# Optimization experiments

Measured on AMD Instinct MI355X. Metric: run time of the kernel, lower is better.

## Reference

```python
import jax, jax.numpy as jnp
import numpy as np

K = 6  # kernel size (square)
_LP = (K - 1) // 2          # 2: PyTorch 'same' left pad for even kernel
_RP = (K - 1) - _LP         # 3: right pad


@jax.custom_vjp
def spike_boxcar(x):
    # Heaviside step with boxcar surrogate gradient (DECOLLE-style)
    return (x > 0).astype(x.dtype)

def _spike_fwd(x):
    return spike_boxcar(x), x

def _spike_bwd(x, g):
    # grad is passed through only where -0.5 < x <= 0.5
    return (jnp.where((x > -0.5) & (x <= 0.5), g, jnp.zeros_like(g)),)

spike_boxcar.defvjp(_spike_fwd, _spike_bwd)


def setup_inputs() -> dict:
    key = jax.random.key(0)
    kx, kw = jax.random.split(key)
    B, Cin, H, W, T = 32, 1, 64, 64, 100
    Cout = 8
    x = jax.random.normal(kx, (B, Cin, H, W, T), dtype=jnp.float32)
    # Conv2d default init: U(-1/sqrt(fan_in), 1/sqrt(fan_in)), fan_in = Cin*K*K
    bound = 1.0 / np.sqrt(Cin * K * K)
    w = jax.random.uniform(kw, (Cout, Cin, K, K), dtype=jnp.float32,
                           minval=-bound, maxval=bound)
    thresh = jnp.full((1,), 0.8, dtype=jnp.float32)
    return {"x": x, "w": w, "thresh": thresh}


def reference(x, w, thresh):
    B, Cin, H, W, T = x.shape
    Cout = w.shape[0]
    # Batch all timesteps into one conv call (conv is independent of state)
    xt = jnp.moveaxis(x, -1, 0).reshape(T * B, Cin, H, W)
    Wx = jax.lax.conv_general_dilated(
        xt, w, window_strides=(1, 1),
        padding=[(_LP, _RP), (_LP, _RP)],
        dimension_numbers=("NCHW", "OIHW", "NCHW"),
    ).reshape(T, B, Cout, H, W)

    ut0 = jnp.zeros((B, Cout, H, W), dtype=x.dtype)
    st0 = jnp.zeros_like(ut0)

    def step(carry, wx):
        ut, st = carry
        ut = ut - st * thresh[0] + wx
        st = spike_boxcar(ut)
        return (ut, st), st

    _, s = jax.lax.scan(step, (ut0, st0), Wx)  # s: [T, B, Cout, H, W]
    return jnp.moveaxis(s, 0, -1)              # [B, Cout, H, W, T]
```

## Files before the change

kernel.cpp:

```cpp
#include <hip/hip_runtime.h>

#define HH 64
#define WW 64
#define TT 100
#define CO 8
#define COB 4
#define KS 6
#define LP 2
#define HALO 21
#define NSITE 441
#define NGMAX 7

__device__ __forceinline__ float stepu(float u, float s, float th, float wx) {
    return __fadd_rn(__fsub_rn(u, __fmul_rn(s, th)), wx);
}

template<int T0, int TC>
__device__ __forceinline__ void process_chunk(
    const float* __restrict__ xb,
    float4* __restrict__ xs, const float (*wds)[CO],
    int tid, int r, int c, int h0, int w0, int co0, float th,
    float* ut, float* sprev, unsigned* bw )
{
    constexpr int NG = TC / 4;

    for (int i = tid; i < NSITE * NG; i += 256) {
        const int s  = i / NG;
        const int tg = i - s * NG;
        const int hr = s / HALO;
        const int hc = s - hr * HALO;
        const int hh = h0 - LP + hr;
        const int ww = w0 - LP + hc;
        float4 v = make_float4(0.f, 0.f, 0.f, 0.f);
        if ((unsigned)hh < (unsigned)HH && (unsigned)ww < (unsigned)WW)
            v = *(const float4*)(xb + ((size_t)hh * WW + ww) * TT + T0 + tg * 4);
        xs[tg * NSITE + s] = v;
    }
    __syncthreads();

    unsigned cb[COB];
#pragma unroll
    for (int j = 0; j < COB; ++j) cb[j] = 0u;

    for (int tg = 0; tg < NG; ++tg) {
        float4 wx[COB];
#pragma unroll
        for (int j = 0; j < COB; ++j) wx[j] = make_float4(0.f, 0.f, 0.f, 0.f);
#pragma unroll
        for (int kh = 0; kh < KS; ++kh) {
#pragma unroll
            for (int kw = 0; kw < KS; ++kw) {
                const float4 xv = xs[tg * NSITE + (r + kh) * HALO + (c + kw)];
                const int tap = kh * KS + kw;
#pragma unroll
                for (int j = 0; j < COB; ++j) {
                    const float wd = wds[tap][co0 + j];
                    wx[j].x = __fmaf_rn(wd, xv.x, wx[j].x);
                    wx[j].y = __fmaf_rn(wd, xv.y, wx[j].y);
                    wx[j].z = __fmaf_rn(wd, xv.z, wx[j].z);
                    wx[j].w = __fmaf_rn(wd, xv.w, wx[j].w);
                }
            }
        }
        const int sh = tg * 4;
#pragma unroll
        for (int j = 0; j < COB; ++j) {
            float u = ut[j], s = sprev[j];
            unsigned m = 0u;
            u = stepu(u, s, th, wx[j].x); s = (u > 0.f) ? 1.f : 0.f; m |= (u > 0.f) ? 1u : 0u;
            u = stepu(u, s, th, wx[j].y); s = (u > 0.f) ? 1.f : 0.f; m |= (u > 0.f) ? 2u : 0u;
            u = stepu(u, s, th, wx[j].z); s = (u > 0.f) ? 1.f : 0.f; m |= (u > 0.f) ? 4u : 0u;
            u = stepu(u, s, th, wx[j].w); s = (u > 0.f) ? 1.f : 0.f; m |= (u > 0.f) ? 8u : 0u;
            ut[j] = u; sprev[j] = s;
            cb[j] |= m << sh;
        }
    }
    __syncthreads();

    constexpr int W0 = T0 / 32;
    constexpr int S  = T0 % 32;
#pragma unroll
    for (int j = 0; j < COB; ++j) {
        bw[j * 4 + W0] |= cb[j] << S;
        if constexpr (S + TC > 32)
            bw[j * 4 + W0 + 1] |= cb[j] >> ((32 - S) & 31);
    }
}

__global__ __launch_bounds__(256, 2)
void sconv2d_spike_kernel(const float* __restrict__ x,
                          const float* __restrict__ wgt,
                          const float* __restrict__ thresh,
                          float* __restrict__ out)
{
    __shared__ float4   xs[NGMAX * NSITE];
    __shared__ float    wds[KS * KS][CO];
    __shared__ unsigned stg[256][5];

    const int tid = threadIdx.x;
    for (int i = tid; i < KS * KS * CO; i += 256) {
        const int co  = i / (KS * KS);
        const int tap = i - co * (KS * KS);
        wds[tap][co] = wgt[co * (KS * KS) + tap];
    }
    const float th = thresh[0];

    const int blk  = blockIdx.x;
    const int b    = blk >> 5;
    const int rest = blk & 31;
    const int tb   = rest >> 1;
    const int co0  = (rest & 1) * COB;
    const int h0   = (tb >> 2) << 4;
    const int w0   = (tb & 3) << 4;
    const int r    = tid >> 4;
    const int c    = tid & 15;

    const float* xb   = x   + (size_t)b * (HH * WW * TT);
    float*       outb = out + (size_t)b * (CO * HH * WW * TT);

    float ut[COB], sprev[COB];
    unsigned bw[COB * 4];
#pragma unroll
    for (int j = 0; j < COB; ++j) { ut[j] = 0.f; sprev[j] = 0.f; }
#pragma unroll
    for (int i = 0; i < COB * 4; ++i) bw[i] = 0u;

    process_chunk< 0, 28>(xb, xs, wds, tid, r, c, h0, w0, co0, th, ut, sprev, bw);
    process_chunk<28, 28>(xb, xs, wds, tid, r, c, h0, w0, co0, th, ut, sprev, bw);
    process_chunk<56, 28>(xb, xs, wds, tid, r, c, h0, w0, co0, th, ut, sprev, bw);
    process_chunk<84, 16>(xb, xs, wds, tid, r, c, h0, w0, co0, th, ut, sprev, bw);

#pragma unroll
    for (int j = 0; j < COB; ++j) {
        const int co = co0 + j;
        stg[tid][0] = bw[j * 4 + 0];
        stg[tid][1] = bw[j * 4 + 1];
        stg[tid][2] = bw[j * 4 + 2];
        stg[tid][3] = bw[j * 4 + 3];
        __syncthreads();
#pragma unroll
        for (int k = 0; k < 25; ++k) {
            const int idx = tid + k * 256;
            const int u   = idx / 25;
            const int tt  = (idx - u * 25) * 4;
            const unsigned bs = stg[u][tt >> 5] >> (tt & 31);
            float4 v;
            v.x = (float)( bs        & 1u);
            v.y = (float)((bs >> 1)  & 1u);
            v.z = (float)((bs >> 2)  & 1u);
            v.w = (float)((bs >> 3)  & 1u);
            const int rr = u >> 4, cc = u & 15;
            *(float4*)(outb + (((size_t)co * HH + (h0 + rr)) * WW + (w0 + cc)) * TT + tt) = v;
        }
        __syncthreads();
    }
}

extern "C" void kernel_launch(void* const* d_in, const int* in_sizes, int n_in,
                              void* d_out, int out_size, void* d_ws, size_t ws_size,
                              hipStream_t stream) {
    const float* x      = (const float*)d_in[0];
    const float* wgt    = (const float*)d_in[1];
    const float* thresh = (const float*)d_in[2];
    float* out = (float*)d_out;

    dim3 grid(32 * 16 * 2);
    dim3 block(256);
    sconv2d_spike_kernel<<<grid, block, 0, stream>>>(x, wgt, thresh, out);
}
```

Baseline: 548.1 us.

## Double-buffer input via global_load_lds and compute all output channels per block

Each block now handles all 8 output channels, halving the grid and avoiding the duplicate halo loads of the old two-channel-group split. Input chunks of 20 timesteps are staged with asynchronous global-to-LDS loads into two ping-pong buffers, so the next chunk's transfer overlaps the current chunk's convolution. Out-of-bounds halo sites are handled by clamped addresses plus per-thread row and column validity masks multiplied into the inputs, instead of branches. The cost is more registers per thread (8 channel accumulators), fewer blocks to fill the machine, and reuse of the LDS input buffer for spike-bit staging.

Result: slower. 1.098 ms (+100.3%).

```diff
diff --git a/kernel.cpp b/kernel.cpp
--- a/kernel.cpp
+++ b/kernel.cpp
@@ -4,86 +4,92 @@
 #define WW 64
 #define TT 100
 #define CO 8
-#define COB 4
 #define KS 6
 #define LP 2
 #define HALO 21
 #define NSITE 441
-#define NGMAX 7
+#define NG 5
+#define SLOT_PAD 2304
 
 __device__ __forceinline__ float stepu(float u, float s, float th, float wx) {
     return __fadd_rn(__fsub_rn(u, __fmul_rn(s, th)), wx);
 }
 
-template<int T0, int TC>
-__device__ __forceinline__ void process_chunk(
-    const float* __restrict__ xb,
-    float4* __restrict__ xs, const float (*wds)[CO],
-    int tid, int r, int c, int h0, int w0, int co0, float th,
-    float* ut, float* sprev, unsigned* bw )
+#define GLDS16(gp, lp) \
+    __builtin_amdgcn_global_load_lds((const __attribute__((address_space(1))) void*)(gp), \
+                                     (__attribute__((address_space(3))) void*)(lp), 16, 0, 0)
+
+__device__ __forceinline__ void stage_chunk(const float* __restrict__ xb,
+                                            float4* __restrict__ dst,
+                                            const int* __restrict__ offs,
+                                            int tid, int t0)
 {
-    constexpr int NG = TC / 4;
-
-    for (int i = tid; i < NSITE * NG; i += 256) {
-        const int s  = i / NG;
-        const int tg = i - s * NG;
-        const int hr = s / HALO;
-        const int hc = s - hr * HALO;
-        const int hh = h0 - LP + hr;
-        const int ww = w0 - LP + hc;
-        float4 v = make_float4(0.f, 0.f, 0.f, 0.f);
-        if ((unsigned)hh < (unsigned)HH && (unsigned)ww < (unsigned)WW)
-            v = *(const float4*)(xb + ((size_t)hh * WW + ww) * TT + T0 + tg * 4);
-        xs[tg * NSITE + s] = v;
-    }
-    __syncthreads();
-
-    unsigned cb[COB];
-#pragma unroll
-    for (int j = 0; j < COB; ++j) cb[j] = 0u;
-
+#pragma unroll
+    for (int k = 0; k < 9; ++k) {
+        GLDS16(xb + offs[k] + t0, dst + tid + k * 256);
+    }
+}
+
+#define FMA4(ACC, WD) \
+    ACC.x = __fmaf_rn((WD), xv.x, ACC.x); \
+    ACC.y = __fmaf_rn((WD), xv.y, ACC.y); \
+    ACC.z = __fmaf_rn((WD), xv.z, ACC.z); \
+    ACC.w = __fmaf_rn((WD), xv.w, ACC.w);
+
+#define SCAN4(J) { \
+    float u = ut[J], s = sprev[J]; unsigned m = 0u; \
+    u = stepu(u, s, th, wx[J].x); s = (u > 0.f) ? 1.f : 0.f; m |= (u > 0.f) ? 1u : 0u; \
+    u = stepu(u, s, th, wx[J].y); s = (u > 0.f) ? 1.f : 0.f; m |= (u > 0.f) ? 2u : 0u; \
+    u = stepu(u, s, th, wx[J].z); s = (u > 0.f) ? 1.f : 0.f; m |= (u > 0.f) ? 4u : 0u; \
+    u = stepu(u, s, th, wx[J].w); s = (u > 0.f) ? 1.f : 0.f; m |= (u > 0.f) ? 8u : 0u; \
+    ut[J] = u; sprev[J] = s; cb[J] |= m << sh; }
+
+template<int T0>
+__device__ __forceinline__ void compute_chunk(
+    const float4* __restrict__ xsb, const float4 (*__restrict__ wds4)[2],
+    int base, float th, const float* __restrict__ vr, const float* __restrict__ vc,
+    float* ut, float* sprev, unsigned* bw)
+{
+    unsigned cb[CO];
+#pragma unroll
+    for (int j = 0; j < CO; ++j) cb[j] = 0u;
+
+#pragma unroll 1
     for (int tg = 0; tg < NG; ++tg) {
-        float4 wx[COB];
-#pragma unroll
-        for (int j = 0; j < COB; ++j) wx[j] = make_float4(0.f, 0.f, 0.f, 0.f);
+        float4 wx[CO];
+#pragma unroll
+        for (int j = 0; j < CO; ++j) wx[j] = make_float4(0.f, 0.f, 0.f, 0.f);
 #pragma unroll
         for (int kh = 0; kh < KS; ++kh) {
 #pragma unroll
             for (int kw = 0; kw < KS; ++kw) {
-                const float4 xv = xs[tg * NSITE + (r + kh) * HALO + (c + kw)];
                 const int tap = kh * KS + kw;
-#pragma unroll
-                for (int j = 0; j < COB; ++j) {
-                    const float wd = wds[tap][co0 + j];
-                    wx[j].x = __fmaf_rn(wd, xv.x, wx[j].x);
-                    wx[j].y = __fmaf_rn(wd, xv.y, wx[j].y);
-                    wx[j].z = __fmaf_rn(wd, xv.z, wx[j].z);
-                    wx[j].w = __fmaf_rn(wd, xv.w, wx[j].w);
-                }
+                float4 xv = xsb[base + (kh * HALO + kw) * NG + tg];
+                const float f = __fmul_rn(vr[kh], vc[kw]);
+                xv.x = __fmul_rn(xv.x, f);
+                xv.y = __fmul_rn(xv.y, f);
+                xv.z = __fmul_rn(xv.z, f);
+                xv.w = __fmul_rn(xv.w, f);
+                const float4 wa = wds4[tap][0];
+                const float4 wb = wds4[tap][1];
+                FMA4(wx[0], wa.x); FMA4(wx[1], wa.y);
+                FMA4(wx[2], wa.z); FMA4(wx[3], wa.w);
+                FMA4(wx[4], wb.x); FMA4(wx[5], wb.y);
+                FMA4(wx[6], wb.z); FMA4(wx[7], wb.w);
             }
         }
         const int sh = tg * 4;
-#pragma unroll
-        for (int j = 0; j < COB; ++j) {
-            float u = ut[j], s = sprev[j];
-            unsigned m = 0u;
-            u = stepu(u, s, th, wx[j].x); s = (u > 0.f) ? 1.f : 0.f; m |= (u > 0.f) ? 1u : 0u;
-            u = stepu(u, s, th, wx[j].y); s = (u > 0.f) ? 1.f : 0.f; m |= (u > 0.f) ? 2u : 0u;
-            u = stepu(u, s, th, wx[j].z); s = (u > 0.f) ? 1.f : 0.f; m |= (u > 0.f) ? 4u : 0u;
-            u = stepu(u, s, th, wx[j].w); s = (u > 0.f) ? 1.f : 0.f; m |= (u > 0.f) ? 8u : 0u;
-            ut[j] = u; sprev[j] = s;
-            cb[j] |= m << sh;
-        }
-    }
-    __syncthreads();
+        SCAN4(0); SCAN4(1); SCAN4(2); SCAN4(3);
+        SCAN4(4); SCAN4(5); SCAN4(6); SCAN4(7);
+    }
 
     constexpr int W0 = T0 / 32;
     constexpr int S  = T0 % 32;
 #pragma unroll
-    for (int j = 0; j < COB; ++j) {
+    for (int j = 0; j < CO; ++j) {
         bw[j * 4 + W0] |= cb[j] << S;
-        if constexpr (S + TC > 32)
-            bw[j * 4 + W0 + 1] |= cb[j] >> ((32 - S) & 31);
+        if constexpr (S + 20 > 32)
+            bw[j * 4 + W0 + 1] |= cb[j] >> (32 - S);
     }
 }
 
@@ -93,66 +99,104 @@
                           const float* __restrict__ thresh,
                           float* __restrict__ out)
 {
-    __shared__ float4   xs[NGMAX * NSITE];
-    __shared__ float    wds[KS * KS][CO];
-    __shared__ unsigned stg[256][5];
+    __shared__ float4 xs[2][SLOT_PAD];
+    __shared__ float4 wds4[KS * KS][2];
 
     const int tid = threadIdx.x;
     for (int i = tid; i < KS * KS * CO; i += 256) {
         const int co  = i / (KS * KS);
         const int tap = i - co * (KS * KS);
-        wds[tap][co] = wgt[co * (KS * KS) + tap];
+        ((float*)wds4)[tap * 8 + co] = wgt[i];
     }
     const float th = thresh[0];
 
-    const int blk  = blockIdx.x;
-    const int b    = blk >> 5;
-    const int rest = blk & 31;
-    const int tb   = rest >> 1;
-    const int co0  = (rest & 1) * COB;
-    const int h0   = (tb >> 2) << 4;
-    const int w0   = (tb & 3) << 4;
-    const int r    = tid >> 4;
-    const int c    = tid & 15;
-
-    const float* xb   = x   + (size_t)b * (HH * WW * TT);
-    float*       outb = out + (size_t)b * (CO * HH * WW * TT);
-
-    float ut[COB], sprev[COB];
-    unsigned bw[COB * 4];
-#pragma unroll
-    for (int j = 0; j < COB; ++j) { ut[j] = 0.f; sprev[j] = 0.f; }
-#pragma unroll
-    for (int i = 0; i < COB * 4; ++i) bw[i] = 0u;
-
-    process_chunk< 0, 28>(xb, xs, wds, tid, r, c, h0, w0, co0, th, ut, sprev, bw);
-    process_chunk<28, 28>(xb, xs, wds, tid, r, c, h0, w0, co0, th, ut, sprev, bw);
-    process_chunk<56, 28>(xb, xs, wds, tid, r, c, h0, w0, co0, th, ut, sprev, bw);
-    process_chunk<84, 16>(xb, xs, wds, tid, r, c, h0, w0, co0, th, ut, sprev, bw);
-
-#pragma unroll
-    for (int j = 0; j < COB; ++j) {
-        const int co = co0 + j;
-        stg[tid][0] = bw[j * 4 + 0];
-        stg[tid][1] = bw[j * 4 + 1];
-        stg[tid][2] = bw[j * 4 + 2];
-        stg[tid][3] = bw[j * 4 + 3];
-        __syncthreads();
+    const int blk = blockIdx.x;
+    const int b   = blk >> 4;
+    const int tb  = blk & 15;
+    const int h0  = (tb >> 2) << 4;
+    const int w0  = (tb & 3) << 4;
+    const int r   = tid >> 4;
+    const int c   = tid & 15;
+
+    const float* xb = x + (size_t)b * (HH * WW * TT);
+
+    int offs[9];
+#pragma unroll
+    for (int k = 0; k < 9; ++k) {
+        const int i = tid + k * 256;
+        int s  = i / NG;
+        int tg = i - s * NG;
+        if (s >= NSITE) { s = NSITE - 1; tg = 0; }
+        const int hr = s / HALO;
+        const int hc = s - hr * HALO;
+        int hh = h0 - LP + hr; hh = hh < 0 ? 0 : (hh > HH - 1 ? HH - 1 : hh);
+        int ww = w0 - LP + hc; ww = ww < 0 ? 0 : (ww > WW - 1 ? WW - 1 : ww);
+        offs[k] = (hh * WW + ww) * TT + tg * 4;
+    }
+
+    float vr[KS], vc[KS];
+#pragma unroll
+    for (int kk = 0; kk < KS; ++kk) {
+        vr[kk] = ((unsigned)(h0 - LP + r + kk) < (unsigned)HH) ? 1.f : 0.f;
+        vc[kk] = ((unsigned)(w0 - LP + c + kk) < (unsigned)WW) ? 1.f : 0.f;
+    }
+
+    float ut[CO], sprev[CO];
+    unsigned bw[CO * 4];
+#pragma unroll
+    for (int j = 0; j < CO; ++j) { ut[j] = 0.f; sprev[j] = 0.f; }
+#pragma unroll
+    for (int i = 0; i < CO * 4; ++i) bw[i] = 0u;
+
+    const int base = (r * HALO + c) * NG;
+
+    stage_chunk(xb, xs[0], offs, tid, 0);
+    __syncthreads();
+
+    stage_chunk(xb, xs[1], offs, tid, 20);
+    compute_chunk< 0>(xs[0], wds4, base, th, vr, vc, ut, sprev, bw);
+    __syncthreads();
+
+    stage_chunk(xb, xs[0], offs, tid, 40);
+    compute_chunk<20>(xs[1], wds4, base, th, vr, vc, ut, sprev, bw);
+    __syncthreads();
+
+    stage_chunk(xb, xs[1], offs, tid, 60);
+    compute_chunk<40>(xs[0], wds4, base, th, vr, vc, ut, sprev, bw);
+    __syncthreads();
+
+    stage_chunk(xb, xs[0], offs, tid, 80);
+    compute_chunk<60>(xs[1], wds4, base, th, vr, vc, ut, sprev, bw);
+    __syncthreads();
+
+    compute_chunk<80>(xs[0], wds4, base, th, vr, vc, ut, sprev, bw);
+    __syncthreads();
+
+    float* outb = out + (size_t)b * (CO * HH * WW * TT);
+    unsigned* stg = (unsigned*)&xs[0][0];
+#pragma unroll
+    for (int j = 0; j < CO; ++j) {
+#pragma unroll
+        for (int w = 0; w < 4; ++w)
+            stg[j * 1280 + tid * 5 + w] = bw[j * 4 + w];
+    }
+    __syncthreads();
+#pragma unroll
+    for (int j = 0; j < CO; ++j) {
 #pragma unroll
         for (int k = 0; k < 25; ++k) {
             const int idx = tid + k * 256;
             const int u   = idx / 25;
             const int tt  = (idx - u * 25) * 4;
-            const unsigned bs = stg[u][tt >> 5] >> (tt & 31);
+            const unsigned bs = stg[j * 1280 + u * 5 + (tt >> 5)] >> (tt & 31);
             float4 v;
             v.x = (float)( bs        & 1u);
             v.y = (float)((bs >> 1)  & 1u);
             v.z = (float)((bs >> 2)  & 1u);
             v.w = (float)((bs >> 3)  & 1u);
             const int rr = u >> 4, cc = u & 15;
-            *(float4*)(outb + (((size_t)co * HH + (h0 + rr)) * WW + (w0 + cc)) * TT + tt) = v;
+            *(float4*)(outb + (((size_t)j * HH + (h0 + rr)) * WW + (w0 + cc)) * TT + tt) = v;
         }
-        __syncthreads();
     }
 }
 
@@ -163,8 +207,7 @@
     const float* wgt    = (const float*)d_in[1];
     const float* thresh = (const float*)d_in[2];
     float* out = (float*)d_out;
-
-    dim3 grid(32 * 16 * 2);
-    dim3 block(256);
-    sconv2d_spike_kernel<<<grid, block, 0, stream>>>(x, wgt, thresh, out);
-}
+    (void)d_ws; (void)ws_size;
+
+    sconv2d_spike_kernel<<<dim3(32 * 16), dim3(256), 0, stream>>>(x, wgt, thresh, out);
+}
```
